# Kernel optimization log

Hardware: AMD Instinct MI355X
Metric: run time of the kernel (lower is better)

Reference implementation:

```python
import jax, jax.numpy as jnp
import numpy as np

N_NODES = 100000
N_EDGES = 3200000
D_FEAT = 128
N_CLASSES = 8


def setup_inputs() -> dict:
    key = jax.random.key(0)
    ks = jax.random.split(key, 8)
    x = jax.random.normal(ks[0], (N_NODES, D_FEAT), dtype=jnp.float32)
    edge_index = jax.random.randint(ks[1], (2, N_EDGES), 0, N_NODES, dtype=jnp.int64)
    W1 = jax.random.normal(ks[2], (D_FEAT, 32), dtype=jnp.float32) / np.sqrt(D_FEAT)
    b1 = jnp.zeros((32,), dtype=jnp.float32)
    W2 = jax.random.normal(ks[3], (32, 16), dtype=jnp.float32) / np.sqrt(32)
    b2 = jnp.zeros((16,), dtype=jnp.float32)
    Wc = jax.random.normal(ks[4], (16, N_CLASSES), dtype=jnp.float32) / np.sqrt(16)
    bc = jnp.zeros((N_CLASSES,), dtype=jnp.float32)
    return {"x": x, "edge_index": edge_index, "W1": W1, "b1": b1,
            "W2": W2, "b2": b2, "Wc": Wc, "bc": bc}


def _gcn_conv(h, src, dst, norm, W, b, num_nodes):
    # PyG GCNConv: linear transform, then sym-normalized scatter-add, then bias
    h = h @ W                                   # [N, out]
    msg = h[src] * norm[:, None]                # [E+N, out] gather + scale
    out = jax.ops.segment_sum(msg, dst, num_segments=num_nodes)
    return out + b


def reference(x, edge_index, W1, b1, W2, b2, Wc, bc):
    num_nodes = x.shape[0]
    loop = jnp.arange(num_nodes, dtype=edge_index.dtype)
    src = jnp.concatenate([edge_index[0], loop])  # add self-loops (PyG default)
    dst = jnp.concatenate([edge_index[1], loop])
    deg = jax.ops.segment_sum(jnp.ones_like(dst, dtype=x.dtype), dst,
                              num_segments=num_nodes)
    dinv = jnp.where(deg > 0, jax.lax.rsqrt(deg), 0.0)
    norm = dinv[src] * dinv[dst]                # symmetric normalization per edge

    h = _gcn_conv(x, src, dst, norm, W1, b1, num_nodes)
    h = jax.nn.relu(h)
    # dropout p=0.5 is identity in eval mode (training=False)
    h = _gcn_conv(h, src, dst, norm, W2, b2, num_nodes)
    h = jax.nn.relu(h)
    logits = h @ Wc + bc
    return jax.nn.log_softmax(logits, axis=1)
```

## Files before the change

kernel.cpp:

```cpp
#include <hip/hip_runtime.h>
#include <math.h>

#define N_NODES 100000
#define N_EDGES 3200000
#define D_FEAT 128
#define H1 32
#define H2 16
#define NC 8

#define NBUCK 391
#define BCAP 16384
#define EPB 8192
#define EPT 16

typedef short s16x8 __attribute__((ext_vector_type(8)));
typedef float f32x4 __attribute__((ext_vector_type(4)));

__device__ inline unsigned short f2bf(float f) {
    unsigned int u = __float_as_uint(f);
    u += 0x7FFF + ((u >> 16) & 1);
    return (unsigned short)(u >> 16);
}
__device__ inline float bf2f(unsigned short h) {
    return __uint_as_float((unsigned int)h << 16);
}


__global__ void k_detect(const int* __restrict__ ei, const float* __restrict__ W1,
                         int* __restrict__ meta, int* __restrict__ bucket_cursor,
                         unsigned short* __restrict__ W1f) {
    __shared__ int red[256];
    int v = 0;
    for (int i = threadIdx.x; i < 1024; i += 256) v |= ei[2 * i + 1];
    red[threadIdx.x] = v;
    __syncthreads();
    for (int s = 128; s > 0; s >>= 1) {
        if (threadIdx.x < (unsigned)s) red[threadIdx.x] |= red[threadIdx.x + s];
        __syncthreads();
    }
    if (threadIdx.x == 0) meta[0] = (red[0] == 0) ? 1 : 0;
    for (int i = threadIdx.x; i < NBUCK; i += 256) bucket_cursor[i] = 0;
    for (int idx = threadIdx.x; idx < 2 * 4 * 64 * 8; idx += 256) {
        const int j    = idx & 7;
        const int lane = (idx >> 3) & 63;
        const int kk   = (idx >> 9) & 3;
        const int nt   = idx >> 11;
        const int k = kk * 32 + ((lane >> 4) << 3) + j;
        const int n = nt * 16 + (lane & 15);
        W1f[idx] = f2bf(W1[k * H1 + n]);
    }
}


__global__ __launch_bounds__(512) void k_bscatter(const int* __restrict__ ei,
                                                  const int* __restrict__ meta,
                                                  int* __restrict__ bucket_cursor,
                                                  int* __restrict__ ebuf) {
    __shared__ int hist[NBUCK];
    __shared__ int lofs[NBUCK];
    __shared__ int rank[NBUCK];
    __shared__ int gb[NBUCK];
    __shared__ int sc[512];
    __shared__ int pay[EPB];
    __shared__ unsigned short pbk[EPB];
    const int tid = threadIdx.x;
    for (int i = tid; i < NBUCK; i += 512) { hist[i] = 0; rank[i] = 0; }
    __syncthreads();
    const int e0 = blockIdx.x * EPB;
    const int n = min(EPB, N_EDGES - e0);
    const bool is64 = (meta[0] != 0);
    int rs[EPT], rd[EPT];
#pragma unroll
    for (int k = 0; k < EPT; ++k) {
        const int i = tid + k * 512;
        if (i < n) {
            const int e = e0 + i;
            if (is64) { rs[k] = ei[2 * e]; rd[k] = ei[2 * N_EDGES + 2 * e]; }
            else      { rs[k] = ei[e];     rd[k] = ei[N_EDGES + e]; }
            atomicAdd(&hist[rd[k] >> 8], 1);
        }
    }
    __syncthreads();
    const int own = (tid < NBUCK) ? hist[tid] : 0;
    sc[tid] = own;
    __syncthreads();
    for (int off = 1; off < 512; off <<= 1) {
        const int v = (tid >= off) ? sc[tid - off] : 0;
        __syncthreads();
        sc[tid] += v;
        __syncthreads();
    }
    if (tid < NBUCK) {
        lofs[tid] = sc[tid] - own;
        if (own > 0) gb[tid] = tid * BCAP + atomicAdd(&bucket_cursor[tid], own);
    }
    __syncthreads();
#pragma unroll
    for (int k = 0; k < EPT; ++k) {
        const int i = tid + k * 512;
        if (i < n) {
            const int b = rd[k] >> 8;
            const int p = lofs[b] + atomicAdd(&rank[b], 1);
            pay[p] = (rs[k] << 8) | (rd[k] & 255);
            pbk[p] = (unsigned short)b;
        }
    }
    __syncthreads();
    for (int p = tid; p < n; p += 512) {
        const int b = pbk[p];
        ebuf[gb[b] + (p - lofs[b])] = pay[p];
    }
}


__global__ __launch_bounds__(512) void k_bscan(const int* __restrict__ bucket_cursor,
                                               int* __restrict__ bucket_base) {
    __shared__ int h[512];
    const int tid = threadIdx.x;
    const int own = (tid < NBUCK) ? bucket_cursor[tid] : 0;
    h[tid] = own;
    __syncthreads();
    for (int off = 1; off < 512; off <<= 1) {
        const int v = (tid >= off) ? h[tid - off] : 0;
        __syncthreads();
        h[tid] += v;
        __syncthreads();
    }
    const int incl = h[tid];
    if (tid < NBUCK) {
        bucket_base[tid] = incl - own;
        if (tid == NBUCK - 1) bucket_base[NBUCK] = incl;
    }
}


__global__ __launch_bounds__(512) void k_bfill2(const int* __restrict__ ebuf,
                                                const int* __restrict__ bucket_base,
                                                int* __restrict__ row_ptr,
                                                float* __restrict__ dinv,
                                                int* __restrict__ col_idx) {
    __shared__ int cnt[256];
    __shared__ int sc[256];
    __shared__ int cur[256];
    const int b = blockIdx.x;
    const int tid = threadIdx.x;
    if (tid < 256) cnt[tid] = 0;
    __syncthreads();
    const int wb = bucket_base[b];
    const int nb = bucket_base[b + 1] - wb;
    const int rb = b * BCAP;
    for (int i = tid; i < nb; i += 512)
        atomicAdd(&cnt[ebuf[rb + i] & 255], 1);
    __syncthreads();
    int own = 0;
    if (tid < 256) { own = cnt[tid]; sc[tid] = own; }
    __syncthreads();
    for (int off = 1; off < 256; off <<= 1) {
        const int v = (tid < 256 && tid >= off) ? sc[tid - off] : 0;
        __syncthreads();
        if (tid < 256) sc[tid] += v;
        __syncthreads();
    }
    if (tid < 256) {
        const int excl = sc[tid] - own;
        const int v = (b << 8) + tid;
        if (v <= N_NODES) row_ptr[v] = wb + excl;
        if (v < N_NODES) dinv[v] = rsqrtf(1.0f + (float)own);
        cur[tid] = wb + excl;
    }
    __syncthreads();
    for (int i = tid; i < nb; i += 512) {
        const int pk = ebuf[rb + i];
        const int slot = atomicAdd(&cur[pk & 255], 1);
        col_idx[slot] = pk >> 8;
    }
}


__global__ __launch_bounds__(256) void k_gemm1m(const float* __restrict__ x,
                                                const unsigned short* __restrict__ W1f,
                                                const float* __restrict__ dinv,
                                                unsigned int* __restrict__ u1q) {
    __shared__ float os[4][16][33];
    const int tid = threadIdx.x;
    const int w = tid >> 6;
    const int lane = tid & 63;
    const int row0 = (blockIdx.x * 4 + w) * 16;
    const bool act = (row0 < N_NODES);
    if (act) {
        const int m = lane & 15;
        const int quad = lane >> 4;
        const s16x8* bf = (const s16x8*)W1f;
        f32x4 acc0 = {0.f, 0.f, 0.f, 0.f};
        f32x4 acc1 = {0.f, 0.f, 0.f, 0.f};
#pragma unroll
        for (int kk = 0; kk < 4; ++kk) {
            const float* xp = x + (size_t)(row0 + m) * D_FEAT + kk * 32 + quad * 8;
            const float4 p0 = ((const float4*)xp)[0];
            const float4 p1 = ((const float4*)xp)[1];
            s16x8 a;
            a[0] = (short)f2bf(p0.x); a[1] = (short)f2bf(p0.y);
            a[2] = (short)f2bf(p0.z); a[3] = (short)f2bf(p0.w);
            a[4] = (short)f2bf(p1.x); a[5] = (short)f2bf(p1.y);
            a[6] = (short)f2bf(p1.z); a[7] = (short)f2bf(p1.w);
            acc0 = __builtin_amdgcn_mfma_f32_16x16x32_bf16(a, bf[kk * 64 + lane], acc0, 0, 0, 0);
            acc1 = __builtin_amdgcn_mfma_f32_16x16x32_bf16(a, bf[(4 + kk) * 64 + lane], acc1, 0, 0, 0);
        }
#pragma unroll
        for (int r = 0; r < 4; ++r) {
            os[w][quad * 4 + r][m]      = acc0[r];
            os[w][quad * 4 + r][16 + m] = acc1[r];
        }
    }
    __syncthreads();
    if (act) {
        const int rl = lane >> 2;
        const int seg = lane & 3;
        const int row = row0 + rl;
        const float dv = dinv[row];
        const float* p = &os[w][rl][seg * 8];
        unsigned int pk0 = __builtin_amdgcn_cvt_pk_fp8_f32(p[0] * dv, p[1] * dv, 0u, false);
        pk0 = __builtin_amdgcn_cvt_pk_fp8_f32(p[2] * dv, p[3] * dv, pk0, true);
        unsigned int pk1 = __builtin_amdgcn_cvt_pk_fp8_f32(p[4] * dv, p[5] * dv, 0u, false);
        pk1 = __builtin_amdgcn_cvt_pk_fp8_f32(p[6] * dv, p[7] * dv, pk1, true);
        uint2 o; o.x = pk0; o.y = pk1;
        ((uint2*)u1q)[(size_t)row * 4 + seg] = o;
    }
}


__global__ __launch_bounds__(256) void k_pull1f(const int* __restrict__ row_ptr,
                                                const int* __restrict__ col_idx,
                                                const float* __restrict__ dinv,
                                                const unsigned int* __restrict__ u1q,
                                                const float* __restrict__ b1,
                                                const float* __restrict__ W2,
                                                unsigned int* __restrict__ u2b) {
    __shared__ float Ws[H1 * H2];
    __shared__ float hs[64][33];
    const int tid = threadIdx.x;
    for (int i = tid; i < H1 * H2; i += 256) Ws[i] = W2[i];
    const int n = tid >> 2;
    const int lq = tid & 3;
    const int v = blockIdx.x * 64 + n;
    float dv = 0.0f;
    if (v < N_NODES) {
        const uint2* base = (const uint2*)u1q;
        uint2 q = base[(size_t)v * 4 + lq];
        float a0 = __builtin_amdgcn_cvt_f32_fp8(q.x, 0);
        float a1 = __builtin_amdgcn_cvt_f32_fp8(q.x, 1);
        float a2 = __builtin_amdgcn_cvt_f32_fp8(q.x, 2);
        float a3 = __builtin_amdgcn_cvt_f32_fp8(q.x, 3);
        float a4 = __builtin_amdgcn_cvt_f32_fp8(q.y, 0);
        float a5 = __builtin_amdgcn_cvt_f32_fp8(q.y, 1);
        float a6 = __builtin_amdgcn_cvt_f32_fp8(q.y, 2);
        float a7 = __builtin_amdgcn_cvt_f32_fp8(q.y, 3);
        const int beg = row_ptr[v];
        const int end = row_ptr[v + 1];
        int i = beg;
        for (; i + 4 <= end; i += 4) {
            const int s0 = col_idx[i + 0];
            const int s1 = col_idx[i + 1];
            const int s2 = col_idx[i + 2];
            const int s3 = col_idx[i + 3];
            const uint2 q0 = base[(size_t)s0 * 4 + lq];
            const uint2 q1 = base[(size_t)s1 * 4 + lq];
            const uint2 q2 = base[(size_t)s2 * 4 + lq];
            const uint2 q3 = base[(size_t)s3 * 4 + lq];
            a0 += __builtin_amdgcn_cvt_f32_fp8(q0.x, 0) + __builtin_amdgcn_cvt_f32_fp8(q1.x, 0)
                + __builtin_amdgcn_cvt_f32_fp8(q2.x, 0) + __builtin_amdgcn_cvt_f32_fp8(q3.x, 0);
            a1 += __builtin_amdgcn_cvt_f32_fp8(q0.x, 1) + __builtin_amdgcn_cvt_f32_fp8(q1.x, 1)
                + __builtin_amdgcn_cvt_f32_fp8(q2.x, 1) + __builtin_amdgcn_cvt_f32_fp8(q3.x, 1);
            a2 += __builtin_amdgcn_cvt_f32_fp8(q0.x, 2) + __builtin_amdgcn_cvt_f32_fp8(q1.x, 2)
                + __builtin_amdgcn_cvt_f32_fp8(q2.x, 2) + __builtin_amdgcn_cvt_f32_fp8(q3.x, 2);
            a3 += __builtin_amdgcn_cvt_f32_fp8(q0.x, 3) + __builtin_amdgcn_cvt_f32_fp8(q1.x, 3)
                + __builtin_amdgcn_cvt_f32_fp8(q2.x, 3) + __builtin_amdgcn_cvt_f32_fp8(q3.x, 3);
            a4 += __builtin_amdgcn_cvt_f32_fp8(q0.y, 0) + __builtin_amdgcn_cvt_f32_fp8(q1.y, 0)
                + __builtin_amdgcn_cvt_f32_fp8(q2.y, 0) + __builtin_amdgcn_cvt_f32_fp8(q3.y, 0);
            a5 += __builtin_amdgcn_cvt_f32_fp8(q0.y, 1) + __builtin_amdgcn_cvt_f32_fp8(q1.y, 1)
                + __builtin_amdgcn_cvt_f32_fp8(q2.y, 1) + __builtin_amdgcn_cvt_f32_fp8(q3.y, 1);
            a6 += __builtin_amdgcn_cvt_f32_fp8(q0.y, 2) + __builtin_amdgcn_cvt_f32_fp8(q1.y, 2)
                + __builtin_amdgcn_cvt_f32_fp8(q2.y, 2) + __builtin_amdgcn_cvt_f32_fp8(q3.y, 2);
            a7 += __builtin_amdgcn_cvt_f32_fp8(q0.y, 3) + __builtin_amdgcn_cvt_f32_fp8(q1.y, 3)
                + __builtin_amdgcn_cvt_f32_fp8(q2.y, 3) + __builtin_amdgcn_cvt_f32_fp8(q3.y, 3);
        }
        for (; i < end; ++i) {
            const int s = col_idx[i];
            const uint2 qq = base[(size_t)s * 4 + lq];
            a0 += __builtin_amdgcn_cvt_f32_fp8(qq.x, 0);
            a1 += __builtin_amdgcn_cvt_f32_fp8(qq.x, 1);
            a2 += __builtin_amdgcn_cvt_f32_fp8(qq.x, 2);
            a3 += __builtin_amdgcn_cvt_f32_fp8(qq.x, 3);
            a4 += __builtin_amdgcn_cvt_f32_fp8(qq.y, 0);
            a5 += __builtin_amdgcn_cvt_f32_fp8(qq.y, 1);
            a6 += __builtin_amdgcn_cvt_f32_fp8(qq.y, 2);
            a7 += __builtin_amdgcn_cvt_f32_fp8(qq.y, 3);
        }
        dv = dinv[v];
        const float4 bb0 = ((const float4*)b1)[lq * 2];
        const float4 bb1 = ((const float4*)b1)[lq * 2 + 1];
        float* hp = &hs[n][lq * 8];
        hp[0] = fmaxf(fmaf(a0, dv, bb0.x), 0.0f);
        hp[1] = fmaxf(fmaf(a1, dv, bb0.y), 0.0f);
        hp[2] = fmaxf(fmaf(a2, dv, bb0.z), 0.0f);
        hp[3] = fmaxf(fmaf(a3, dv, bb0.w), 0.0f);
        hp[4] = fmaxf(fmaf(a4, dv, bb1.x), 0.0f);
        hp[5] = fmaxf(fmaf(a5, dv, bb1.y), 0.0f);
        hp[6] = fmaxf(fmaf(a6, dv, bb1.z), 0.0f);
        hp[7] = fmaxf(fmaf(a7, dv, bb1.w), 0.0f);
    }
    __syncthreads();
    if (v < N_NODES) {
        const int j0 = lq * 4;
        float s0 = 0.f, s1 = 0.f, s2 = 0.f, s3 = 0.f;
#pragma unroll
        for (int k = 0; k < H1; ++k) {
            const float hk = hs[n][k];
            s0 = fmaf(hk, Ws[k * H2 + j0 + 0], s0);
            s1 = fmaf(hk, Ws[k * H2 + j0 + 1], s1);
            s2 = fmaf(hk, Ws[k * H2 + j0 + 2], s2);
            s3 = fmaf(hk, Ws[k * H2 + j0 + 3], s3);
        }
        uint2 o;
        o.x = (unsigned int)f2bf(s0 * dv) | ((unsigned int)f2bf(s1 * dv) << 16);
        o.y = (unsigned int)f2bf(s2 * dv) | ((unsigned int)f2bf(s3 * dv) << 16);
        ((uint2*)u2b)[(size_t)v * 4 + lq] = o;
    }
}


__global__ __launch_bounds__(256) void k_pull2f(const int* __restrict__ row_ptr,
                                                const int* __restrict__ col_idx,
                                                const float* __restrict__ dinv,
                                                const unsigned int* __restrict__ u2b,
                                                const float* __restrict__ b2,
                                                const float* __restrict__ Wc,
                                                const float* __restrict__ bc,
                                                float* __restrict__ out) {
    __shared__ float hs[64][17];
    __shared__ float Wcs[H2 * NC];
    __shared__ float bcs[NC];
    const int tid = threadIdx.x;
    if (tid < H2 * NC) Wcs[tid] = Wc[tid];
    if (tid < NC) bcs[tid] = bc[tid];
    const int n = tid >> 2;
    const int lq = tid & 3;
    const int v = blockIdx.x * 64 + n;
    if (v < N_NODES) {
        const uint2* base = (const uint2*)u2b;
        uint2 q = base[(size_t)v * 4 + lq];
        float a0 = bf2f((unsigned short)q.x), a1 = bf2f((unsigned short)(q.x >> 16));
        float a2 = bf2f((unsigned short)q.y), a3 = bf2f((unsigned short)(q.y >> 16));
        const int beg = row_ptr[v];
        const int end = row_ptr[v + 1];
        int i = beg;
        for (; i + 4 <= end; i += 4) {
            const int s0 = col_idx[i + 0];
            const int s1 = col_idx[i + 1];
            const int s2 = col_idx[i + 2];
            const int s3 = col_idx[i + 3];
            const uint2 q0 = base[(size_t)s0 * 4 + lq];
            const uint2 q1 = base[(size_t)s1 * 4 + lq];
            const uint2 q2 = base[(size_t)s2 * 4 + lq];
            const uint2 q3 = base[(size_t)s3 * 4 + lq];
            a0 += bf2f((unsigned short)q0.x) + bf2f((unsigned short)q1.x)
                + bf2f((unsigned short)q2.x) + bf2f((unsigned short)q3.x);
            a1 += bf2f((unsigned short)(q0.x >> 16)) + bf2f((unsigned short)(q1.x >> 16))
                + bf2f((unsigned short)(q2.x >> 16)) + bf2f((unsigned short)(q3.x >> 16));
            a2 += bf2f((unsigned short)q0.y) + bf2f((unsigned short)q1.y)
                + bf2f((unsigned short)q2.y) + bf2f((unsigned short)q3.y);
            a3 += bf2f((unsigned short)(q0.y >> 16)) + bf2f((unsigned short)(q1.y >> 16))
                + bf2f((unsigned short)(q2.y >> 16)) + bf2f((unsigned short)(q3.y >> 16));
        }
        for (; i < end; ++i) {
            const int s = col_idx[i];
            const uint2 qq = base[(size_t)s * 4 + lq];
            a0 += bf2f((unsigned short)qq.x); a1 += bf2f((unsigned short)(qq.x >> 16));
            a2 += bf2f((unsigned short)qq.y); a3 += bf2f((unsigned short)(qq.y >> 16));
        }
        const float dv = dinv[v];
        const float4 bb = ((const float4*)b2)[lq];
        float* hp = &hs[n][lq * 4];
        hp[0] = fmaxf(fmaf(a0, dv, bb.x), 0.0f);
        hp[1] = fmaxf(fmaf(a1, dv, bb.y), 0.0f);
        hp[2] = fmaxf(fmaf(a2, dv, bb.z), 0.0f);
        hp[3] = fmaxf(fmaf(a3, dv, bb.w), 0.0f);
    }
    __syncthreads();
    if (tid < 64) {
        const int vv = blockIdx.x * 64 + tid;
        if (vv < N_NODES) {
            float lg[NC];
#pragma unroll
            for (int j = 0; j < NC; ++j) lg[j] = bcs[j];
#pragma unroll
            for (int k = 0; k < H2; ++k) {
                const float hk = hs[tid][k];
#pragma unroll
                for (int j = 0; j < NC; ++j)
                    lg[j] = fmaf(hk, Wcs[k * NC + j], lg[j]);
            }
            float m = lg[0];
#pragma unroll
            for (int j = 1; j < NC; ++j) m = fmaxf(m, lg[j]);
            float s = 0.0f;
#pragma unroll
            for (int j = 0; j < NC; ++j) s += expf(lg[j] - m);
            const float lse = logf(s) + m;
            float4 o0, o1;
            o0.x = lg[0] - lse; o0.y = lg[1] - lse;
            o0.z = lg[2] - lse; o0.w = lg[3] - lse;
            o1.x = lg[4] - lse; o1.y = lg[5] - lse;
            o1.z = lg[6] - lse; o1.w = lg[7] - lse;
            float4* op = (float4*)(out + (size_t)vv * NC);
            op[0] = o0; op[1] = o1;
        }
    }
}


extern "C" void kernel_launch(void* const* d_in, const int* in_sizes, int n_in,
                              void* d_out, int out_size, void* d_ws, size_t ws_size,
                              hipStream_t stream) {
    const float* x   = (const float*)d_in[0];
    const int*   ei  = (const int*)d_in[1];
    const float* W1  = (const float*)d_in[2];
    const float* b1  = (const float*)d_in[3];
    const float* W2  = (const float*)d_in[4];
    const float* b2  = (const float*)d_in[5];
    const float* Wc  = (const float*)d_in[6];
    const float* bc  = (const float*)d_in[7];
    float* out = (float*)d_out;

    int*   meta          = (int*)d_ws;
    int*   bucket_cursor = meta + 16;
    int*   bucket_base   = bucket_cursor + 512;
    int*   row_ptr       = bucket_base + 512;
    float* dinv          = (float*)(row_ptr + 100016);
    unsigned short* W1f  = (unsigned short*)(dinv + 100000);
    int*   col_idx       = (int*)W1f + 2048;
    int*   ebuf          = col_idx + 3200000;
    unsigned int* u1q    = (unsigned int*)ebuf;
    unsigned int* u2b    = (unsigned int*)(ebuf + NBUCK * BCAP);

    k_detect  <<<1, 256, 0, stream>>>(ei, W1, meta, bucket_cursor, W1f);
    k_bscatter<<<(N_EDGES + EPB - 1) / EPB, 512, 0, stream>>>(ei, meta, bucket_cursor, ebuf);
    k_bscan   <<<1, 512, 0, stream>>>(bucket_cursor, bucket_base);
    k_bfill2  <<<NBUCK, 512, 0, stream>>>(ebuf, bucket_base, row_ptr, dinv, col_idx);

    k_gemm1m<<<(N_NODES + 63) / 64, 256, 0, stream>>>(x, W1f, dinv, u1q);
    k_pull1f<<<(N_NODES + 63) / 64, 256, 0, stream>>>(row_ptr, col_idx, dinv, u1q, b1, W2, u2b);
    k_pull2f<<<(N_NODES + 63) / 64, 256, 0, stream>>>(row_ptr, col_idx, dinv, u2b, b2, Wc, bc, out);
}
```

Measured before the change: 223.2 us.

## Vectorize edge loads, fuse bucket scan into fill, stage col_idx in LDS, shuffle indices

The bucket scatter kernel now processes half as many edges per block and loads source and destination indices with vector loads. The separate bucket-scan kernel is removed and every fill block redoes the small prefix scan over bucket counts itself. The fill kernel sorts column indices into a shared-memory buffer and writes them out contiguously, so global stores become coalesced. Both pull kernels load column indices cooperatively across the four lanes of a node and broadcast them with shuffles, unrolled to eight neighbours, to cut redundant index loads. The costs are one less kernel launch traded for redundant scan work in each fill block, and 64KB of LDS per fill block.

Result: faster. 209.8 us (-6.0%).

```diff
diff --git a/kernel.cpp b/kernel.cpp
--- a/kernel.cpp
+++ b/kernel.cpp
@@ -10,8 +10,8 @@
 
 #define NBUCK 391
 #define BCAP 16384
-#define EPB 8192
-#define EPT 16
+#define EPB 4096
+#define EPT 8
 
 typedef short s16x8 __attribute__((ext_vector_type(8)));
 typedef float f32x4 __attribute__((ext_vector_type(4)));
@@ -70,14 +70,33 @@
     const int n = min(EPB, N_EDGES - e0);
     const bool is64 = (meta[0] != 0);
     int rs[EPT], rd[EPT];
-#pragma unroll
-    for (int k = 0; k < EPT; ++k) {
-        const int i = tid + k * 512;
-        if (i < n) {
-            const int e = e0 + i;
-            if (is64) { rs[k] = ei[2 * e]; rd[k] = ei[2 * N_EDGES + 2 * e]; }
-            else      { rs[k] = ei[e];     rd[k] = ei[N_EDGES + e]; }
-            atomicAdd(&hist[rd[k] >> 8], 1);
+    if (is64) {
+#pragma unroll
+        for (int k = 0; k < EPT / 2; ++k) {
+            const int i = 2 * (tid + k * 512);
+            if (i < n) {
+                const int e = e0 + i;
+                const int4 s = *(const int4*)&ei[2 * e];
+                const int4 d = *(const int4*)&ei[2 * N_EDGES + 2 * e];
+                rs[2 * k] = s.x; rs[2 * k + 1] = s.z;
+                rd[2 * k] = d.x; rd[2 * k + 1] = d.z;
+                atomicAdd(&hist[d.x >> 8], 1);
+                atomicAdd(&hist[d.z >> 8], 1);
+            }
+        }
+    } else {
+#pragma unroll
+        for (int k = 0; k < EPT / 2; ++k) {
+            const int i = 2 * (tid + k * 512);
+            if (i < n) {
+                const int e = e0 + i;
+                const int2 s = *(const int2*)&ei[e];
+                const int2 d = *(const int2*)&ei[N_EDGES + e];
+                rs[2 * k] = s.x; rs[2 * k + 1] = s.y;
+                rd[2 * k] = d.x; rd[2 * k + 1] = d.y;
+                atomicAdd(&hist[d.x >> 8], 1);
+                atomicAdd(&hist[d.y >> 8], 1);
+            }
         }
     }
     __syncthreads();
@@ -96,13 +115,16 @@
     }
     __syncthreads();
 #pragma unroll
-    for (int k = 0; k < EPT; ++k) {
-        const int i = tid + k * 512;
+    for (int k = 0; k < EPT / 2; ++k) {
+        const int i = 2 * (tid + k * 512);
         if (i < n) {
-            const int b = rd[k] >> 8;
-            const int p = lofs[b] + atomicAdd(&rank[b], 1);
-            pay[p] = (rs[k] << 8) | (rd[k] & 255);
-            pbk[p] = (unsigned short)b;
+#pragma unroll
+            for (int j = 0; j < 2; ++j) {
+                const int b = rd[2 * k + j] >> 8;
+                const int p = lofs[b] + atomicAdd(&rank[b], 1);
+                pay[p] = (rs[2 * k + j] << 8) | (rd[2 * k + j] & 255);
+                pbk[p] = (unsigned short)b;
+            }
         }
     }
     __syncthreads();
@@ -113,41 +135,33 @@
 }
 
 
-__global__ __launch_bounds__(512) void k_bscan(const int* __restrict__ bucket_cursor,
-                                               int* __restrict__ bucket_base) {
-    __shared__ int h[512];
-    const int tid = threadIdx.x;
-    const int own = (tid < NBUCK) ? bucket_cursor[tid] : 0;
-    h[tid] = own;
-    __syncthreads();
-    for (int off = 1; off < 512; off <<= 1) {
-        const int v = (tid >= off) ? h[tid - off] : 0;
-        __syncthreads();
-        h[tid] += v;
-        __syncthreads();
-    }
-    const int incl = h[tid];
-    if (tid < NBUCK) {
-        bucket_base[tid] = incl - own;
-        if (tid == NBUCK - 1) bucket_base[NBUCK] = incl;
-    }
-}
-
-
 __global__ __launch_bounds__(512) void k_bfill2(const int* __restrict__ ebuf,
-                                                const int* __restrict__ bucket_base,
+                                                const int* __restrict__ bucket_cursor,
                                                 int* __restrict__ row_ptr,
                                                 float* __restrict__ dinv,
                                                 int* __restrict__ col_idx) {
+    __shared__ int h[512];
     __shared__ int cnt[256];
     __shared__ int sc[256];
     __shared__ int cur[256];
+    __shared__ int srt[BCAP];
+    __shared__ int s_wb, s_nb;
     const int b = blockIdx.x;
     const int tid = threadIdx.x;
+    const int own0 = (tid < NBUCK) ? bucket_cursor[tid] : 0;
+    h[tid] = own0;
     if (tid < 256) cnt[tid] = 0;
     __syncthreads();
-    const int wb = bucket_base[b];
-    const int nb = bucket_base[b + 1] - wb;
+    for (int off = 1; off < 512; off <<= 1) {
+        const int v = (tid >= off) ? h[tid - off] : 0;
+        __syncthreads();
+        h[tid] += v;
+        __syncthreads();
+    }
+    if (tid == b) { s_wb = h[tid] - own0; s_nb = own0; }
+    __syncthreads();
+    const int wb = s_wb;
+    const int nb = s_nb;
     const int rb = b * BCAP;
     for (int i = tid; i < nb; i += 512)
         atomicAdd(&cnt[ebuf[rb + i] & 255], 1);
@@ -166,14 +180,17 @@
         const int v = (b << 8) + tid;
         if (v <= N_NODES) row_ptr[v] = wb + excl;
         if (v < N_NODES) dinv[v] = rsqrtf(1.0f + (float)own);
-        cur[tid] = wb + excl;
+        cur[tid] = excl;
     }
     __syncthreads();
     for (int i = tid; i < nb; i += 512) {
         const int pk = ebuf[rb + i];
         const int slot = atomicAdd(&cur[pk & 255], 1);
-        col_idx[slot] = pk >> 8;
-    }
+        srt[slot] = pk >> 8;
+    }
+    __syncthreads();
+    for (int i = tid; i < nb; i += 512)
+        col_idx[wb + i] = srt[i];
 }
 
 
@@ -229,6 +246,17 @@
 }
 
 
+#define ACC8(Q) do { \
+    a0 += __builtin_amdgcn_cvt_f32_fp8((Q).x, 0); \
+    a1 += __builtin_amdgcn_cvt_f32_fp8((Q).x, 1); \
+    a2 += __builtin_amdgcn_cvt_f32_fp8((Q).x, 2); \
+    a3 += __builtin_amdgcn_cvt_f32_fp8((Q).x, 3); \
+    a4 += __builtin_amdgcn_cvt_f32_fp8((Q).y, 0); \
+    a5 += __builtin_amdgcn_cvt_f32_fp8((Q).y, 1); \
+    a6 += __builtin_amdgcn_cvt_f32_fp8((Q).y, 2); \
+    a7 += __builtin_amdgcn_cvt_f32_fp8((Q).y, 3); \
+} while (0)
+
 __global__ __launch_bounds__(256) void k_pull1f(const int* __restrict__ row_ptr,
                                                 const int* __restrict__ col_idx,
                                                 const float* __restrict__ dinv,
@@ -242,6 +270,7 @@
     for (int i = tid; i < H1 * H2; i += 256) Ws[i] = W2[i];
     const int n = tid >> 2;
     const int lq = tid & 3;
+    const int lb = (tid & 63) & ~3;
     const int v = blockIdx.x * 64 + n;
     float dv = 0.0f;
     if (v < N_NODES) {
@@ -258,43 +287,44 @@
         const int beg = row_ptr[v];
         const int end = row_ptr[v + 1];
         int i = beg;
-        for (; i + 4 <= end; i += 4) {
-            const int s0 = col_idx[i + 0];
-            const int s1 = col_idx[i + 1];
-            const int s2 = col_idx[i + 2];
-            const int s3 = col_idx[i + 3];
+        for (; i + 8 <= end; i += 8) {
+            const int c0 = col_idx[i + lq];
+            const int c1 = col_idx[i + 4 + lq];
+            const int s0 = __shfl(c0, lb + 0, 64);
+            const int s1 = __shfl(c0, lb + 1, 64);
+            const int s2 = __shfl(c0, lb + 2, 64);
+            const int s3 = __shfl(c0, lb + 3, 64);
+            const int s4 = __shfl(c1, lb + 0, 64);
+            const int s5 = __shfl(c1, lb + 1, 64);
+            const int s6 = __shfl(c1, lb + 2, 64);
+            const int s7 = __shfl(c1, lb + 3, 64);
             const uint2 q0 = base[(size_t)s0 * 4 + lq];
             const uint2 q1 = base[(size_t)s1 * 4 + lq];
             const uint2 q2 = base[(size_t)s2 * 4 + lq];
             const uint2 q3 = base[(size_t)s3 * 4 + lq];
-            a0 += __builtin_amdgcn_cvt_f32_fp8(q0.x, 0) + __builtin_amdgcn_cvt_f32_fp8(q1.x, 0)
-                + __builtin_amdgcn_cvt_f32_fp8(q2.x, 0) + __builtin_amdgcn_cvt_f32_fp8(q3.x, 0);
-            a1 += __builtin_amdgcn_cvt_f32_fp8(q0.x, 1) + __builtin_amdgcn_cvt_f32_fp8(q1.x, 1)
-                + __builtin_amdgcn_cvt_f32_fp8(q2.x, 1) + __builtin_amdgcn_cvt_f32_fp8(q3.x, 1);
-            a2 += __builtin_amdgcn_cvt_f32_fp8(q0.x, 2) + __builtin_amdgcn_cvt_f32_fp8(q1.x, 2)
-                + __builtin_amdgcn_cvt_f32_fp8(q2.x, 2) + __builtin_amdgcn_cvt_f32_fp8(q3.x, 2);
-            a3 += __builtin_amdgcn_cvt_f32_fp8(q0.x, 3) + __builtin_amdgcn_cvt_f32_fp8(q1.x, 3)
-                + __builtin_amdgcn_cvt_f32_fp8(q2.x, 3) + __builtin_amdgcn_cvt_f32_fp8(q3.x, 3);
-            a4 += __builtin_amdgcn_cvt_f32_fp8(q0.y, 0) + __builtin_amdgcn_cvt_f32_fp8(q1.y, 0)
-                + __builtin_amdgcn_cvt_f32_fp8(q2.y, 0) + __builtin_amdgcn_cvt_f32_fp8(q3.y, 0);
-            a5 += __builtin_amdgcn_cvt_f32_fp8(q0.y, 1) + __builtin_amdgcn_cvt_f32_fp8(q1.y, 1)
-                + __builtin_amdgcn_cvt_f32_fp8(q2.y, 1) + __builtin_amdgcn_cvt_f32_fp8(q3.y, 1);
-            a6 += __builtin_amdgcn_cvt_f32_fp8(q0.y, 2) + __builtin_amdgcn_cvt_f32_fp8(q1.y, 2)
-                + __builtin_amdgcn_cvt_f32_fp8(q2.y, 2) + __builtin_amdgcn_cvt_f32_fp8(q3.y, 2);
-            a7 += __builtin_amdgcn_cvt_f32_fp8(q0.y, 3) + __builtin_amdgcn_cvt_f32_fp8(q1.y, 3)
-                + __builtin_amdgcn_cvt_f32_fp8(q2.y, 3) + __builtin_amdgcn_cvt_f32_fp8(q3.y, 3);
+            const uint2 q4 = base[(size_t)s4 * 4 + lq];
+            const uint2 q5 = base[(size_t)s5 * 4 + lq];
+            const uint2 q6 = base[(size_t)s6 * 4 + lq];
+            const uint2 q7 = base[(size_t)s7 * 4 + lq];
+            ACC8(q0); ACC8(q1); ACC8(q2); ACC8(q3);
+            ACC8(q4); ACC8(q5); ACC8(q6); ACC8(q7);
+        }
+        for (; i + 4 <= end; i += 4) {
+            const int c0 = col_idx[i + lq];
+            const int s0 = __shfl(c0, lb + 0, 64);
+            const int s1 = __shfl(c0, lb + 1, 64);
+            const int s2 = __shfl(c0, lb + 2, 64);
+            const int s3 = __shfl(c0, lb + 3, 64);
+            const uint2 q0 = base[(size_t)s0 * 4 + lq];
+            const uint2 q1 = base[(size_t)s1 * 4 + lq];
+            const uint2 q2 = base[(size_t)s2 * 4 + lq];
+            const uint2 q3 = base[(size_t)s3 * 4 + lq];
+            ACC8(q0); ACC8(q1); ACC8(q2); ACC8(q3);
         }
         for (; i < end; ++i) {
             const int s = col_idx[i];
             const uint2 qq = base[(size_t)s * 4 + lq];
-            a0 += __builtin_amdgcn_cvt_f32_fp8(qq.x, 0);
-            a1 += __builtin_amdgcn_cvt_f32_fp8(qq.x, 1);
-            a2 += __builtin_amdgcn_cvt_f32_fp8(qq.x, 2);
-            a3 += __builtin_amdgcn_cvt_f32_fp8(qq.x, 3);
-            a4 += __builtin_amdgcn_cvt_f32_fp8(qq.y, 0);
-            a5 += __builtin_amdgcn_cvt_f32_fp8(qq.y, 1);
-            a6 += __builtin_amdgcn_cvt_f32_fp8(qq.y, 2);
-            a7 += __builtin_amdgcn_cvt_f32_fp8(qq.y, 3);
+            ACC8(qq);
         }
         dv = dinv[v];
         const float4 bb0 = ((const float4*)b1)[lq * 2];
@@ -328,6 +358,13 @@
     }
 }
 
+
+#define ACC4(Q) do { \
+    a0 += bf2f((unsigned short)(Q).x); \
+    a1 += bf2f((unsigned short)((Q).x >> 16)); \
+    a2 += bf2f((unsigned short)(Q).y); \
+    a3 += bf2f((unsigned short)((Q).y >> 16)); \
+} while (0)
 
 __global__ __launch_bounds__(256) void k_pull2f(const int* __restrict__ row_ptr,
                                                 const int* __restrict__ col_idx,
@@ -345,6 +382,7 @@
     if (tid < NC) bcs[tid] = bc[tid];
     const int n = tid >> 2;
     const int lq = tid & 3;
+    const int lb = (tid & 63) & ~3;
     const int v = blockIdx.x * 64 + n;
     if (v < N_NODES) {
         const uint2* base = (const uint2*)u2b;
@@ -354,29 +392,44 @@
         const int beg = row_ptr[v];
         const int end = row_ptr[v + 1];
         int i = beg;
-        for (; i + 4 <= end; i += 4) {
-            const int s0 = col_idx[i + 0];
-            const int s1 = col_idx[i + 1];
-            const int s2 = col_idx[i + 2];
-            const int s3 = col_idx[i + 3];
+        for (; i + 8 <= end; i += 8) {
+            const int c0 = col_idx[i + lq];
+            const int c1 = col_idx[i + 4 + lq];
+            const int s0 = __shfl(c0, lb + 0, 64);
+            const int s1 = __shfl(c0, lb + 1, 64);
+            const int s2 = __shfl(c0, lb + 2, 64);
+            const int s3 = __shfl(c0, lb + 3, 64);
+            const int s4 = __shfl(c1, lb + 0, 64);
+            const int s5 = __shfl(c1, lb + 1, 64);
+            const int s6 = __shfl(c1, lb + 2, 64);
+            const int s7 = __shfl(c1, lb + 3, 64);
             const uint2 q0 = base[(size_t)s0 * 4 + lq];
             const uint2 q1 = base[(size_t)s1 * 4 + lq];
             const uint2 q2 = base[(size_t)s2 * 4 + lq];
             const uint2 q3 = base[(size_t)s3 * 4 + lq];
-            a0 += bf2f((unsigned short)q0.x) + bf2f((unsigned short)q1.x)
-                + bf2f((unsigned short)q2.x) + bf2f((unsigned short)q3.x);
-            a1 += bf2f((unsigned short)(q0.x >> 16)) + bf2f((unsigned short)(q1.x >> 16))
-                + bf2f((unsigned short)(q2.x >> 16)) + bf2f((unsigned short)(q3.x >> 16));
-            a2 += bf2f((unsigned short)q0.y) + bf2f((unsigned short)q1.y)
-                + bf2f((unsigned short)q2.y) + bf2f((unsigned short)q3.y);
-            a3 += bf2f((unsigned short)(q0.y >> 16)) + bf2f((unsigned short)(q1.y >> 16))
-                + bf2f((unsigned short)(q2.y >> 16)) + bf2f((unsigned short)(q3.y >> 16));
+            const uint2 q4 = base[(size_t)s4 * 4 + lq];
+            const uint2 q5 = base[(size_t)s5 * 4 + lq];
+            const uint2 q6 = base[(size_t)s6 * 4 + lq];
+            const uint2 q7 = base[(size_t)s7 * 4 + lq];
+            ACC4(q0); ACC4(q1); ACC4(q2); ACC4(q3);
+            ACC4(q4); ACC4(q5); ACC4(q6); ACC4(q7);
+        }
+        for (; i + 4 <= end; i += 4) {
+            const int c0 = col_idx[i + lq];
+            const int s0 = __shfl(c0, lb + 0, 64);
+            const int s1 = __shfl(c0, lb + 1, 64);
+            const int s2 = __shfl(c0, lb + 2, 64);
+            const int s3 = __shfl(c0, lb + 3, 64);
+            const uint2 q0 = base[(size_t)s0 * 4 + lq];
+            const uint2 q1 = base[(size_t)s1 * 4 + lq];
+            const uint2 q2 = base[(size_t)s2 * 4 + lq];
+            const uint2 q3 = base[(size_t)s3 * 4 + lq];
+            ACC4(q0); ACC4(q1); ACC4(q2); ACC4(q3);
         }
         for (; i < end; ++i) {
             const int s = col_idx[i];
             const uint2 qq = base[(size_t)s * 4 + lq];
-            a0 += bf2f((unsigned short)qq.x); a1 += bf2f((unsigned short)(qq.x >> 16));
-            a2 += bf2f((unsigned short)qq.y); a3 += bf2f((unsigned short)(qq.y >> 16));
+            ACC4(qq);
         }
         const float dv = dinv[v];
         const float4 bb = ((const float4*)b2)[lq];
@@ -445,8 +498,7 @@
 
     k_detect  <<<1, 256, 0, stream>>>(ei, W1, meta, bucket_cursor, W1f);
     k_bscatter<<<(N_EDGES + EPB - 1) / EPB, 512, 0, stream>>>(ei, meta, bucket_cursor, ebuf);
-    k_bscan   <<<1, 512, 0, stream>>>(bucket_cursor, bucket_base);
-    k_bfill2  <<<NBUCK, 512, 0, stream>>>(ebuf, bucket_base, row_ptr, dinv, col_idx);
+    k_bfill2  <<<NBUCK, 512, 0, stream>>>(ebuf, bucket_cursor, row_ptr, dinv, col_idx);
 
     k_gemm1m<<<(N_NODES + 63) / 64, 256, 0, stream>>>(x, W1f, dinv, u1q);
     k_pull1f<<<(N_NODES + 63) / 64, 256, 0, stream>>>(row_ptr, col_idx, dinv, u1q, b1, W2, u2b);
```
